# Optimization experiments

Hardware: AMD Instinct MI355X
Metric: run time of the kernel (lower is better)

Reference implementation:

```python
import jax, jax.numpy as jnp
import numpy as np
import math

B, N, D, H, T = 256, 512, 512, 8, 128
HD = D // H
CLIP = 10.0
CAP = 1.0
NEG = -1.0e9


def setup_inputs() -> dict:
    key = jax.random.key(0)
    ks = jax.random.split(key, 12)
    s = 1.0 / math.sqrt(D)
    return {
        "embeddings": jax.random.normal(ks[0], (B, N, D), jnp.float32),
        "mean_graph_emb": jax.random.normal(ks[1], (B, D), jnp.float32),
        "used_capacity": jax.random.uniform(ks[2], (T, B), jnp.float32),
        "Wk": jax.random.normal(ks[3], (D, D), jnp.float32) * s,
        "Wk_tanh": jax.random.normal(ks[4], (D, D), jnp.float32) * s,
        "Wv": jax.random.normal(ks[5], (D, D), jnp.float32) * s,
        "Wq_context": jax.random.normal(ks[6], (D, D), jnp.float32) * s,
        "Wq_step": jax.random.normal(ks[7], (D + 1, D), jnp.float32) * s,
        "Wout": jax.random.normal(ks[8], (D, D), jnp.float32) * s,
        "prev_a": jax.random.randint(ks[9], (T, B), 0, N, jnp.int32),
        "mask": jax.random.randint(ks[10], (T, B, N), 0, 2, jnp.int32),
    }


def reference(embeddings, mean_graph_emb, used_capacity, Wk, Wk_tanh, Wv,
              Wq_context, Wq_step, Wout, prev_a, mask):
    # Projections (done once per graph embedding, as in get_projections)
    K = (embeddings @ Wk).reshape(B, N, H, HD).transpose(0, 2, 1, 3)      # [B,H,N,hd]
    V = (embeddings @ Wv).reshape(B, N, H, HD).transpose(0, 2, 1, 3)      # [B,H,N,hd]
    K_tanh = embeddings @ Wk_tanh                                          # [B,N,D]
    Q_context = mean_graph_emb @ Wq_context                                # [B,D]

    inv_sqrt_hd = 1.0 / math.sqrt(HD)
    inv_sqrt_d = 1.0 / math.sqrt(D)

    def step(carry, xs):
        prev_t, cap_t, mask_t = xs  # [B], [B], [B,N]
        # get_step_context: gather prev node embedding + remaining capacity
        cur_emb = jnp.take_along_axis(embeddings, prev_t[:, None, None], axis=1)[:, 0]  # [B,D]
        step_ctx = jnp.concatenate([cur_emb, (CAP - cap_t)[:, None]], axis=-1)          # [B,D+1]
        q = Q_context + step_ctx @ Wq_step                                               # [B,D]
        qh = q.reshape(B, H, HD)                                                          # [B,H,hd]
        # decoder MHA, seq_len_q = 1
        logits = jnp.einsum("bhd,bhnd->bhn", qh, K) * inv_sqrt_hd                        # [B,H,N]
        logits = jnp.where(mask_t[:, None, :] == 1, NEG, logits)
        attn = jax.nn.softmax(logits, axis=-1)
        mha = jnp.einsum("bhn,bhnd->bhd", attn, V).reshape(B, D) @ Wout                  # [B,D]
        # single-head tanh-clipped pointer logits
        comp = jnp.einsum("bd,bnd->bn", mha, K_tanh) * inv_sqrt_d                        # [B,N]
        comp = jnp.tanh(comp) * CLIP
        comp = jnp.where(mask_t == 1, NEG, comp)
        p = jax.nn.softmax(comp, axis=-1)                                                # [B,N]
        return carry, p

    _, ps = jax.lax.scan(step, None, (prev_a, used_capacity, mask))  # [T,B,N]
    return ps.transpose(1, 0, 2)  # [B,T,N]
```

## Files before the change

### kernel.cpp

```cpp
#include <hip/hip_runtime.h>
#include <hip/hip_bf16.h>

constexpr int Bb = 256;
constexpr int Nn = 512;
constexpr int Dd = 512;
constexpr int Hh = 8;
constexpr int Tt = 128;
#define NEGF (-1.0e9f)

typedef __attribute__((ext_vector_type(4))) float f32x4;
typedef __attribute__((ext_vector_type(8))) short bf16x8;
typedef __attribute__((ext_vector_type(8))) unsigned short u16x8;

#define AS1 __attribute__((address_space(1)))
#define AS3 __attribute__((address_space(3)))

__device__ __forceinline__ unsigned short f2bf(float f) {
  union { float f; unsigned u; } v; v.f = f;
  unsigned r = v.u + 0x7fffu + ((v.u >> 16) & 1u);
  return (unsigned short)(r >> 16);
}

__device__ __forceinline__ unsigned cvtpk(float lo, float hi) {
  unsigned r;
  asm("v_cvt_pk_bf16_f32 %0, %1, %2" : "=v"(r) : "v"(lo), "v"(hi));
  return r;
}

__device__ __forceinline__ void cast8(const float* __restrict__ src,
                                      unsigned short* __restrict__ dst, int i) {
  const float4* s = (const float4*)src + (size_t)i * 2;
  float4 a = s[0], b = s[1];
  u16x8 o;
  o[0] = f2bf(a.x); o[1] = f2bf(a.y); o[2] = f2bf(a.z); o[3] = f2bf(a.w);
  o[4] = f2bf(b.x); o[5] = f2bf(b.y); o[6] = f2bf(b.z); o[7] = f2bf(b.w);
  ((u16x8*)dst)[i] = o;
}

__global__ void prep_k(const float* __restrict__ emb, const int* __restrict__ mask,
                       const float* __restrict__ Wkt, const float* __restrict__ Wout,
                       const float* __restrict__ mge,
                       const float* __restrict__ Wk, const float* __restrict__ Wv,
                       const float* __restrict__ Wqs, const float* __restrict__ Wqc,
                       unsigned short* __restrict__ embB, unsigned* __restrict__ bits,
                       unsigned short* __restrict__ WktB, unsigned short* __restrict__ WoutB,
                       unsigned short* __restrict__ mgeB,
                       unsigned short* __restrict__ WkT, unsigned short* __restrict__ WvT,
                       unsigned short* __restrict__ WqsT, unsigned short* __restrict__ WqcT) {
  __shared__ float t[32][33];
  int bid = blockIdx.x, tid = threadIdx.x;
  if (bid < 32768) {
    cast8(emb, embB, bid * 256 + tid);
  } else if (bid < 98304) {
    size_t gid = (size_t)(bid - 32768) * 256 + tid;
    int mv = mask[gid];
    unsigned long long bal = __ballot(mv == 1);
    if ((tid & 63) == 0) {
      unsigned tt = (unsigned)(gid >> 17);
      unsigned b = (unsigned)((gid >> 9) & 255);
      unsigned n = (unsigned)(gid & 511);
      unsigned* dst = bits + (((size_t)b * 128 + tt) * 16 + (n >> 5));
      dst[0] = (unsigned)bal;
      dst[1] = (unsigned)(bal >> 32);
    }
  } else if (bid < 98432) {
    cast8(Wkt, WktB, (bid - 98304) * 256 + tid);
  } else if (bid < 98560) {
    cast8(Wout, WoutB, (bid - 98432) * 256 + tid);
  } else if (bid < 98624) {
    cast8(mge, mgeB, (bid - 98560) * 256 + tid);
  } else {
    int vb = bid - 98624;
    int mid = vb >> 8;
    int tile = vb & 255;
    const float* S = (mid == 0) ? Wk : (mid == 1) ? Wv : (mid == 2) ? Wqs : Wqc;
    unsigned short* Dst = (mid == 0) ? WkT : (mid == 1) ? WvT : (mid == 2) ? WqsT : WqcT;
    int r0 = (tile >> 4) * 32, c0 = (tile & 15) * 32;
    int tx = tid & 31, ty = tid >> 5;
#pragma unroll
    for (int yy = 0; yy < 4; ++yy) {
      int r = ty + yy * 8;
      t[r][tx] = S[(size_t)(r0 + r) * 512 + c0 + tx];
    }
    __syncthreads();
#pragma unroll
    for (int yy = 0; yy < 4; ++yy) {
      int c = ty + yy * 8;
      Dst[(size_t)(c0 + c) * 512 + r0 + tx] = f2bf(t[tx][c]);
    }
  }
}

__device__ __forceinline__ void stage_tile(const unsigned short* __restrict__ G, int row0, int k0,
                                           unsigned short* lds_base, int wave, int lane) {
#pragma unroll
  for (int c = 0; c < 4; ++c) {
    int chunk = wave * 4 + c;
    const unsigned short* g = G + (size_t)(row0 + chunk * 8 + (lane >> 3)) * 512 + k0 + (lane & 7) * 8;
    __builtin_amdgcn_global_load_lds((AS1 void*)g, (AS3 void*)(lds_base + chunk * 512), 16, 0, 0);
  }
}

__global__ __launch_bounds__(256, 2)
void wfqc_k(const unsigned short* __restrict__ A0, const unsigned short* __restrict__ BT0,
            unsigned short* __restrict__ C0,
            const unsigned short* __restrict__ A1, const unsigned short* __restrict__ BT1,
            float* __restrict__ C1) {
  __shared__ __align__(16) char lds[32768];
  unsigned short* ldsA = (unsigned short*)lds;
  unsigned short* ldsB = ldsA + 8192;
  int bid = blockIdx.x;
  bool qc = (bid >= 16);
  int lb = qc ? bid - 16 : bid;
  const unsigned short* A = qc ? A1 : A0;
  const unsigned short* BT = qc ? BT1 : BT0;
  int mt = lb >> 2, nt = lb & 3;
  int m0 = mt * 128, n0 = nt * 128;
  int tid = threadIdx.x, lane = tid & 63, w = tid >> 6;
  int wm = w >> 1, wn = w & 1;
  int l15 = lane & 15, l4 = lane >> 4;

  f32x4 acc[4][4] = {};
  for (int k0 = 0; k0 < 512; k0 += 64) {
    stage_tile(A, m0, k0, ldsA, w, lane);
    stage_tile(BT, n0, k0, ldsB, w, lane);
    __syncthreads();
#pragma unroll
    for (int ks = 0; ks < 2; ++ks) {
      bf16x8 fa[4], fb[4];
#pragma unroll
      for (int ii = 0; ii < 4; ++ii)
        fa[ii] = *(const bf16x8*)(ldsA + (wm * 64 + ii * 16 + l15) * 64 + ks * 32 + l4 * 8);
#pragma unroll
      for (int jj = 0; jj < 4; ++jj)
        fb[jj] = *(const bf16x8*)(ldsB + (wn * 64 + jj * 16 + l15) * 64 + ks * 32 + l4 * 8);
#pragma unroll
      for (int ii = 0; ii < 4; ++ii)
#pragma unroll
        for (int jj = 0; jj < 4; ++jj)
          acc[ii][jj] = __builtin_amdgcn_mfma_f32_16x16x32_bf16(fa[ii], fb[jj], acc[ii][jj], 0, 0, 0);
    }
    __syncthreads();
  }
#pragma unroll
  for (int ii = 0; ii < 4; ++ii)
#pragma unroll
    for (int jj = 0; jj < 4; ++jj)
#pragma unroll
      for (int r = 0; r < 4; ++r) {
        int row = m0 + wm * 64 + ii * 16 + l4 * 4 + r;
        int col = n0 + wn * 64 + jj * 16 + l15;
        if (qc) C1[(size_t)row * 512 + col] = acc[ii][jj][r];
        else C0[(size_t)row * 512 + col] = f2bf(acc[ii][jj][r]);
      }
}

#define LDA_Q(QM)                                                   \
  _Pragma("unroll")                                                 \
  for (int ii = 0; ii < 4; ++ii) {                                  \
    int rr_ = (QM) * 64 + ii * 16 + l15;                            \
    const char* ap_ = ldsAh + rr_ * 128;                            \
    int sw_ = (rr_ & 7) << 4;                                       \
    fa[ii][0] = *(const bf16x8*)(ap_ + ((l4 * 16) ^ sw_));          \
    fa[ii][1] = *(const bf16x8*)(ap_ + ((64 + l4 * 16) ^ sw_));     \
  }

#define LDB_Q(QN)                                                   \
  _Pragma("unroll")                                                 \
  for (int jj = 0; jj < 2; ++jj) {                                  \
    int rr_ = (wn & 1) * 64 + (QN) * 32 + jj * 16 + l15;            \
    const char* bp_ = ldsBh + rr_ * 128;                            \
    int sw_ = (rr_ & 7) << 4;                                       \
    fb[jj][0] = *(const bf16x8*)(bp_ + ((l4 * 16) ^ sw_));          \
    fb[jj][1] = *(const bf16x8*)(bp_ + ((64 + l4 * 16) ^ sw_));     \
  }

#define MM16(QM, QN)                                                              \
  do {                                                                            \
    __builtin_amdgcn_s_setprio(1);                                                \
    _Pragma("unroll")                                                             \
    for (int ii = 0; ii < 4; ++ii)                                                \
      _Pragma("unroll")                                                           \
      for (int jj = 0; jj < 2; ++jj) {                                            \
        acc[(QM) * 4 + ii][(QN) * 2 + jj] = __builtin_amdgcn_mfma_f32_16x16x32_bf16( \
            fa[ii][0], fb[jj][0], acc[(QM) * 4 + ii][(QN) * 2 + jj], 0, 0, 0);    \
        acc[(QM) * 4 + ii][(QN) * 2 + jj] = __builtin_amdgcn_mfma_f32_16x16x32_bf16( \
            fa[ii][1], fb[jj][1], acc[(QM) * 4 + ii][(QN) * 2 + jj], 0, 0, 0);    \
      }                                                                           \
    __builtin_amdgcn_s_setprio(0);                                                \
  } while (0)

#define STAGE10A(SLOT, H, ROWB, KT)                                               \
  do {                                                                             \
    int rb_ = (ROWB) + (H) * 128;                                                  \
    char* Lb_ = lds + (SLOT) * 32768 + (H) * 16384;                                \
    _Pragma("unroll")                                                              \
    for (int sh_ = 0; sh_ < 2; ++sh_) {                                            \
      int off_ = sh_ * 8192 + tid * 16;                                            \
      int r_ = off_ >> 7;                                                          \
      int c_ = (off_ & 127) ^ ((r_ & 7) << 4);                                     \
      const char* g_ = (const char*)(A + (size_t)(rb_ + r_) * 512 + (KT) * 64) + c_; \
      __builtin_amdgcn_global_load_lds((AS1 void*)g_, (AS3 void*)(Lb_ + off_), 16, 0, 0); \
    }                                                                              \
  } while (0)

#define STAGE10B(SLOT, H, KT)                                                      \
  do {                                                                             \
    int rb_ = n0 + (H) * 128;                                                      \
    char* Lb_ = lds + 98304 + (SLOT) * 32768 + (H) * 16384;                        \
    _Pragma("unroll")                                                              \
    for (int sh_ = 0; sh_ < 2; ++sh_) {                                            \
      int off_ = sh_ * 8192 + tid * 16;                                            \
      int r_ = off_ >> 7;                                                          \
      int c_ = (off_ & 127) ^ ((r_ & 7) << 4);                                     \
      const char* g_ = (const char*)(BT + (size_t)(rb_ + r_) * 512 + (KT) * 64) + c_; \
      __builtin_amdgcn_global_load_lds((AS1 void*)g_, (AS3 void*)(Lb_ + off_), 16, 0, 0); \
    }                                                                              \
  } while (0)

#define STAGE11A(SLOT, H, KT)                                                      \
  do {                                                                             \
    char* Lb_ = lds + (SLOT) * 65536 + (H) * 16384;                                \
    __builtin_amdgcn_global_load_lds((AS1 void*)(abase[(H) * 2 + 0] + (KT) * 128), \
        (AS3 void*)(Lb_ + tid * 16), 16, 0, 0);                                    \
    __builtin_amdgcn_global_load_lds((AS1 void*)(abase[(H) * 2 + 1] + (KT) * 128), \
        (AS3 void*)(Lb_ + 8192 + tid * 16), 16, 0, 0);                             \
  } while (0)

#define STAGE11B(SLOT, H, KT)                                                      \
  do {                                                                             \
    int rb_ = n0 + (H) * 128;                                                      \
    char* Lb_ = lds + (SLOT) * 65536 + 32768 + (H) * 16384;                        \
    _Pragma("unroll")                                                              \
    for (int sh_ = 0; sh_ < 2; ++sh_) {                                            \
      int off_ = sh_ * 8192 + tid * 16;                                            \
      int r_ = off_ >> 7;                                                          \
      int c_ = (off_ & 127) ^ ((r_ & 7) << 4);                                     \
      const char* g_ = (const char*)(BT + (size_t)(rb_ + r_) * 512 + (KT) * 64) + c_; \
      __builtin_amdgcn_global_load_lds((AS1 void*)g_, (AS3 void*)(Lb_ + off_), 16, 0, 0); \
    }                                                                              \
  } while (0)

__global__ __launch_bounds__(512, 1)
void gemmq_k(const unsigned short* __restrict__ embB,
             const unsigned short* __restrict__ WqsT,
             unsigned short* __restrict__ Qb,
             const float* __restrict__ Qc, const float* __restrict__ WqsL,
             const float* __restrict__ capp, const int* __restrict__ prev,
             const unsigned short* __restrict__ B0, const unsigned short* __restrict__ B1,
             unsigned short* __restrict__ C0, unsigned short* __restrict__ C2) {
  __shared__ __align__(16) char lds[163840];
  int tid = threadIdx.x, lane = tid & 63, w = tid >> 6;
  int l15 = lane & 15, l4 = lane >> 4;

  if (blockIdx.x < 256) {
    const unsigned short* A = embB;
    const unsigned short* BT = WqsT;
    int xcd = blockIdx.x & 7, loc = blockIdx.x >> 3;
    int mt = xcd * 16 + (loc >> 1), nh = loc & 1;
    int m0 = mt * 256, n0 = nh * 256;
    int wm = w >> 2, wn = w & 3;

    const char* abase[4];
#pragma unroll
    for (int hs = 0; hs < 4; ++hs) {
      int H = hs >> 1, sh = hs & 1;
      int off = sh * 8192 + tid * 16;
      int r = off >> 7;
      int c = (off & 127) ^ ((r & 7) << 4);
      int row = m0 + H * 128 + r;
      int t = row >> 8, bb = row & 255;
      int pa = prev[t * Bb + bb];
      abase[hs] = (const char*)(A + (size_t)(bb * 512 + pa) * 512) + c;
    }

    f32x4 acc[8][4] = {};
    bf16x8 fa[4][2], fb[2][2];

    STAGE11A(0, 0, 0); STAGE11A(0, 1, 0);
    STAGE11B(0, 0, 0); STAGE11B(0, 1, 0);

    for (int kt = 0; kt < 8; ++kt) {
      int s = kt & 1, sn = s ^ 1;
      char* ldsAh = lds + s * 65536 + wm * 16384;
      char* ldsBh = lds + s * 65536 + 32768 + (wn >> 1) * 16384;
      if (kt < 7) {
        STAGE11A(sn, 0, kt + 1);
        asm volatile("s_waitcnt vmcnt(2)" ::: "memory");
      } else {
        asm volatile("s_waitcnt vmcnt(0)" ::: "memory");
      }
      __builtin_amdgcn_s_barrier();
      LDA_Q(0); LDB_Q(0);
      MM16(0, 0);
      __builtin_amdgcn_s_barrier();
      LDB_Q(1);
      if (kt < 7) STAGE11A(sn, 1, kt + 1);
      __builtin_amdgcn_s_barrier();
      MM16(0, 1);
      __builtin_amdgcn_s_barrier();
      LDA_Q(1);
      if (kt < 7) STAGE11B(sn, 0, kt + 1);
      __builtin_amdgcn_s_barrier();
      MM16(1, 1);
      __builtin_amdgcn_s_barrier();
      LDB_Q(0);
      if (kt < 7) STAGE11B(sn, 1, kt + 1);
      __builtin_amdgcn_s_barrier();
      MM16(1, 0);
      __builtin_amdgcn_s_barrier();
    }

#pragma unroll
    for (int mi = 0; mi < 8; ++mi)
#pragma unroll
      for (int nj = 0; nj < 4; ++nj)
#pragma unroll
        for (int r = 0; r < 4; ++r) {
          int row = m0 + wm * 128 + mi * 16 + l4 * 4 + r;
          int col = n0 + wn * 64 + nj * 16 + l15;
          int t = row >> 8, bbx = row & 255;
          float val = acc[mi][nj][r] + Qc[(size_t)bbx * 512 + col] + (1.0f - capp[row]) * WqsL[col];
          Qb[(size_t)(bbx * 128 + t) * 512 + col] = f2bf(val * 0.125f);
        }
  } else {
    const unsigned short* A = embB;
    int bid = blockIdx.x - 256;
    int xcd = bid & 7, loc = bid >> 3;
    int ml4 = loc >> 2, cmb = loc & 3;
    int grp = cmb >> 1, nh = cmb & 1;
    const unsigned short* BT = grp ? B1 : B0;
    int mtb = xcd * 64 + ml4 * 4;
    int n0 = nh * 256;
    int wm = w >> 2, wn = w & 3;

    f32x4 acc[8][4] = {};
    bf16x8 fa[4][2], fb[2][2];

    {
      int m00 = mtb * 256;
      STAGE10A(0, 0, m00, 0); STAGE10A(0, 1, m00, 0);
      STAGE10A(1, 0, m00, 1); STAGE10A(1, 1, m00, 1);
      STAGE10B(0, 0, 0);      STAGE10B(0, 1, 0);
    }

    for (int g = 0; g < 32; ++g) {
      int As = g % 3, Astg = (g + 2) % 3;
      int Bs = g & 1, Bstg = Bs ^ 1;
      char* ldsAh = lds + As * 32768 + wm * 16384;
      char* ldsBh = lds + 98304 + Bs * 32768 + (wn >> 1) * 16384;
      int g2 = g + 2;
      int m0A = (mtb + (g2 >> 3)) * 256, ktA = g2 & 7;
      int ktB = (g + 1) & 7;
      if (g < 30) {
        STAGE10A(Astg, 0, m0A, ktA);
        asm volatile("s_waitcnt vmcnt(2)" ::: "memory");
      } else {
        asm volatile("s_waitcnt vmcnt(0)" ::: "memory");
      }
      __builtin_amdgcn_s_barrier();
      LDA_Q(0); LDB_Q(0);
      MM16(0, 0);
      __builtin_amdgcn_s_barrier();
      LDB_Q(1);
      if (g < 30) STAGE10A(Astg, 1, m0A, ktA);
      __builtin_amdgcn_s_barrier();
      MM16(0, 1);
      __builtin_amdgcn_s_barrier();
      LDA_Q(1);
      if (g < 31) STAGE10B(Bstg, 0, ktB);
      __builtin_amdgcn_s_barrier();
      MM16(1, 1);
      __builtin_amdgcn_s_barrier();
      LDB_Q(0);
      if (g < 31) STAGE10B(Bstg, 1, ktB);
      __builtin_amdgcn_s_barrier();
      MM16(1, 0);
      __builtin_amdgcn_s_barrier();

      if ((g & 7) == 7) {
        int m0cur = (mtb + (g >> 3)) * 256;
        if (grp == 0) {
#pragma unroll
          for (int mi = 0; mi < 8; ++mi)
#pragma unroll
            for (int nj = 0; nj < 4; ++nj)
#pragma unroll
              for (int r = 0; r < 4; ++r) {
                int row = m0cur + wm * 128 + mi * 16 + l4 * 4 + r;
                int col = n0 + wn * 64 + nj * 16 + l15;
                C0[(size_t)row * 512 + col] = f2bf(acc[mi][nj][r]);
              }
        } else {
          int bb = m0cur >> 9, nn0 = m0cur & 511;
          char* wb = lds + As * 32768 + w * 4096;
          int rdrow = lane >> 3, nseg = lane & 7;
#pragma unroll
          for (int p = 0; p < 8; ++p) {
            int nj = p >> 1;
            if ((l15 >> 3) == (p & 1)) {
              int rowL = l15 & 7;
#pragma unroll
              for (int mi = 0; mi < 8; ++mi) {
                ushort4 w4;
                w4.x = f2bf(acc[mi][nj][0]);
                w4.y = f2bf(acc[mi][nj][1]);
                w4.z = f2bf(acc[mi][nj][2]);
                w4.w = f2bf(acc[mi][nj][3]);
                *(ushort4*)(wb + rowL * 272 + (mi * 16 + l4 * 4) * 2) = w4;
              }
            }
            asm volatile("s_waitcnt lgkmcnt(0)" ::: "memory");
            u16x8 v0 = *(const u16x8*)(wb + rdrow * 272 + nseg * 16);
            u16x8 v1 = *(const u16x8*)(wb + rdrow * 272 + 128 + nseg * 16);
            int dglob = n0 + wn * 64 + p * 8 + rdrow;
            unsigned short* dp = C2 + (size_t)(bb * 512 + dglob) * 512 + nn0 + wm * 128;
            *(u16x8*)(dp + nseg * 8) = v0;
            *(u16x8*)(dp + 64 + nseg * 8) = v1;
            asm volatile("s_waitcnt lgkmcnt(0)" ::: "memory");
          }
        }
#pragma unroll
        for (int mi = 0; mi < 8; ++mi)
#pragma unroll
          for (int nj = 0; nj < 4; ++nj)
            acc[mi][nj] = (f32x4){0.f, 0.f, 0.f, 0.f};
        __syncthreads();
      }
    }
  }
}

__global__ __launch_bounds__(512, 1)
void gemm11_k(const unsigned short* __restrict__ A, const unsigned short* __restrict__ BT,
              unsigned short* __restrict__ C) {
  __shared__ __align__(16) char lds[131072];
  int xcd = blockIdx.x & 7, loc = blockIdx.x >> 3;
  int mt = xcd * 16 + (loc >> 1), nh = loc & 1;
  int m0 = mt * 256, n0 = nh * 256;
  int tid = threadIdx.x, lane = tid & 63, w = tid >> 6;
  int wm = w >> 2, wn = w & 3;
  int l15 = lane & 15, l4 = lane >> 4;

  const char* abase[4];
#pragma unroll
  for (int hs = 0; hs < 4; ++hs) {
    int H = hs >> 1, sh = hs & 1;
    int off = sh * 8192 + tid * 16;
    int r = off >> 7;
    int c = (off & 127) ^ ((r & 7) << 4);
    int row = m0 + H * 128 + r;
    abase[hs] = (const char*)(A + (size_t)row * 512) + c;
  }

  f32x4 acc[8][4] = {};
  bf16x8 fa[4][2], fb[2][2];

  STAGE11A(0, 0, 0); STAGE11A(0, 1, 0);
  STAGE11B(0, 0, 0); STAGE11B(0, 1, 0);

  for (int kt = 0; kt < 8; ++kt) {
    int s = kt & 1, sn = s ^ 1;
    char* ldsAh = lds + s * 65536 + wm * 16384;
    char* ldsBh = lds + s * 65536 + 32768 + (wn >> 1) * 16384;
    if (kt < 7) {
      STAGE11A(sn, 0, kt + 1);
      asm volatile("s_waitcnt vmcnt(2)" ::: "memory");
    } else {
      asm volatile("s_waitcnt vmcnt(0)" ::: "memory");
    }
    __builtin_amdgcn_s_barrier();
    LDA_Q(0); LDB_Q(0);
    MM16(0, 0);
    __builtin_amdgcn_s_barrier();
    LDB_Q(1);
    if (kt < 7) STAGE11A(sn, 1, kt + 1);
    __builtin_amdgcn_s_barrier();
    MM16(0, 1);
    __builtin_amdgcn_s_barrier();
    LDA_Q(1);
    if (kt < 7) STAGE11B(sn, 0, kt + 1);
    __builtin_amdgcn_s_barrier();
    MM16(1, 1);
    __builtin_amdgcn_s_barrier();
    LDB_Q(0);
    if (kt < 7) STAGE11B(sn, 1, kt + 1);
    __builtin_amdgcn_s_barrier();
    MM16(1, 0);
    __builtin_amdgcn_s_barrier();
  }

#pragma unroll
  for (int mi = 0; mi < 8; ++mi)
#pragma unroll
    for (int nj = 0; nj < 4; ++nj)
#pragma unroll
      for (int r = 0; r < 4; ++r) {
        int row = m0 + wm * 128 + mi * 16 + l4 * 4 + r;
        int col = n0 + wn * 64 + nj * 16 + l15;
        C[(size_t)row * 512 + col] = f2bf(acc[mi][nj][r]);
      }
}

#define STAGEK5(CH, SLOT)                                                          \
  do {                                                                             \
    _Pragma("unroll")                                                              \
    for (int sh_ = 0; sh_ < 2; ++sh_) {                                            \
      int off_ = sh_ * 8192 + tid * 16;                                            \
      int r_ = off_ >> 7;                                                          \
      int c_ = (off_ & 127) ^ ((r_ & 7) << 4);                                     \
      const char* g_ = (const char*)(Kb + (size_t)(b * 512 + (CH) * 128 + r_) * 512 + h * 64) + c_; \
      __builtin_amdgcn_global_load_lds((AS1 void*)g_, (AS3 void*)(lds + (SLOT) * 16384 + off_), 16, 0, 0); \
    }                                                                              \
  } while (0)

#define STAGEV5(CH, SLOT)                                                          \
  do {                                                                             \
    _Pragma("unroll")                                                              \
    for (int sh_ = 0; sh_ < 2; ++sh_) {                                            \
      int off_ = sh_ * 8192 + tid * 16;                                            \
      int r_ = off_ >> 8;                                                          \
      int c_ = (off_ & 255) ^ ((r_ & 7) << 4);                                     \
      const char* g_ = (const char*)(Vt + (size_t)(b * 512 + h * 64 + r_) * 512 + (CH) * 128) + c_; \
      __builtin_amdgcn_global_load_lds((AS1 void*)g_, (AS3 void*)(lds + 32768 + (SLOT) * 16384 + off_), 16, 0, 0); \
    }                                                                              \
  } while (0)

#define CHUNK5(CH)                                                                 \
  do {                                                                             \
    const char* Ks_ = lds + ((CH) & 1) * 16384;                                    \
    const char* Vs_ = lds + 32768 + ((CH) & 1) * 16384;                            \
    f32x4 sck[8];                                                                  \
    _Pragma("unroll")                                                              \
    for (int jj = 0; jj < 8; ++jj) sck[jj] = (f32x4){0.f, 0.f, 0.f, 0.f};          \
    _Pragma("unroll")                                                              \
    for (int jj = 0; jj < 8; ++jj) {                                               \
      int rr_ = jj * 16 + l15;                                                     \
      int sw_ = (rr_ & 7) << 4;                                                    \
      bf16x8 k0_ = *(const bf16x8*)(Ks_ + rr_ * 128 + ((l4 * 16) ^ sw_));          \
      bf16x8 k1_ = *(const bf16x8*)(Ks_ + rr_ * 128 + ((64 + l4 * 16) ^ sw_));     \
      sck[jj] = __builtin_amdgcn_mfma_f32_16x16x32_bf16(k0_, fq[0], sck[jj], 0, 0, 0); \
      sck[jj] = __builtin_amdgcn_mfma_f32_16x16x32_bf16(k1_, fq[1], sck[jj], 0, 0, 0); \
    }                                                                              \
    unsigned mwarr_[4] = {mqs[CH].x, mqs[CH].y, mqs[CH].z, mqs[CH].w};             \
    float cmx_ = -3.0e38f;                                                         \
    _Pragma("unroll")                                                              \
    for (int jj = 0; jj < 8; ++jj) {                                               \
      unsigned nib_ = mwarr_[jj >> 1] >> (((jj & 1) << 4) + (l4 << 2));            \
      _Pragma("unroll")                                                            \
      for (int r = 0; r < 4; ++r)                                                  \
        sck[jj][r] = ((nib_ >> r) & 1) ? NEGF : sck[jj][r];                        \
      float m01_ = fmaxf(sck[jj][0], sck[jj][1]);                                  \
      float m23_ = fmaxf(sck[jj][2], sck[jj][3]);                                  \
      cmx_ = fmaxf(cmx_, fmaxf(m01_, m23_));                                       \
    }                                                                              \
    cmx_ = fmaxf(cmx_, __shfl_xor(cmx_, 16));                                      \
    cmx_ = fmaxf(cmx_, __shfl_xor(cmx_, 32));                                      \
    float mn_ = fmaxf(mx, cmx_);                                                   \
    float al_ = __expf(mx - mn_);                                                  \
    sum *= al_;                                                                    \
    _Pragma("unroll")                                                              \
    for (int dj = 0; dj < 4; ++dj)                                                 \
      _Pragma("unroll")                                                            \
      for (int r = 0; r < 4; ++r) o[dj][r] *= al_;                                 \
    mx = mn_;                                                                      \
    _Pragma("unroll")                                                              \
    for (int jj = 0; jj < 8; ++jj) {                                               \
      _Pragma("unroll")                                                            \
      for (int r = 0; r < 4; ++r) sck[jj][r] = __expf(sck[jj][r] - mx);            \
      sum += (sck[jj][0] + sck[jj][1]) + (sck[jj][2] + sck[jj][3]);                \
    }                                                                              \
    _Pragma("unroll")                                                              \
    for (int g = 0; g < 4; ++g) {                                                  \
      unsigned a0_ = cvtpk(sck[2 * g][0], sck[2 * g][1]);                          \
      unsigned a1_ = cvtpk(sck[2 * g][2], sck[2 * g][3]);                          \
      unsigned b0_ = cvtpk(sck[2 * g + 1][0], sck[2 * g + 1][1]);                  \
      unsigned b1_ = cvtpk(sck[2 * g + 1][2], sck[2 * g + 1][3]);                  \
      unsigned wA0_ = __shfl(a0_, src0, 64), wB0_ = __shfl(b0_, src0, 64);         \
      unsigned wA1_ = __shfl(a1_, src0, 64), wB1_ = __shfl(b1_, src0, 64);         \
      unsigned wA2_ = __shfl(a0_, src2, 64), wB2_ = __shfl(b0_, src2, 64);         \
      unsigned wA3_ = __shfl(a1_, src2, 64), wB3_ = __shfl(b1_, src2, 64);         \
      union { unsigned u[4]; bf16x8 v; } pu_;                                      \
      pu_.u[0] = loh ? wA0_ : wB0_;                                                \
      pu_.u[1] = loh ? wA1_ : wB1_;                                                \
      pu_.u[2] = loh ? wA2_ : wB2_;                                                \
      pu_.u[3] = loh ? wA3_ : wB3_;                                                \
      _Pragma("unroll")                                                            \
      for (int dj = 0; dj < 4; ++dj) {                                             \
        int rr_ = dj * 16 + l15;                                                   \
        int sw_ = (rr_ & 7) << 4;                                                  \
        bf16x8 fv_ = *(const bf16x8*)(Vs_ + rr_ * 256 + ((g * 64 + l4 * 16) ^ sw_)); \
        o[dj] = __builtin_amdgcn_mfma_f32_16x16x32_bf16(fv_, pu_.v, o[dj], 0, 0, 0); \
      }                                                                            \
    }                                                                              \
  } while (0)

__global__ __launch_bounds__(512, 4)
void attn5_k(const unsigned short* __restrict__ Qb, const unsigned short* __restrict__ Kb,
             const unsigned short* __restrict__ Vt, const unsigned* __restrict__ mbits,
             unsigned short* __restrict__ mhaB) {
  __shared__ __align__(16) char lds[65536];
  int bid = blockIdx.x;
  int h = bid & 7, b = bid >> 3;
  int tid = threadIdx.x, lane = tid & 63, w = tid >> 6;
  int l15 = lane & 15, l4 = lane >> 4;
  int t = w * 16 + l15;

  bf16x8 fq[2];
#pragma unroll
  for (int ks = 0; ks < 2; ++ks)
    fq[ks] = *(const bf16x8*)(Qb + (size_t)(b * 128 + t) * 512 + h * 64 + ks * 32 + l4 * 8);
  uint4 mqs[4];
  {
    const uint4* mp = (const uint4*)(mbits + (((size_t)b * 128 + t) << 4));
    mqs[0] = mp[0]; mqs[1] = mp[1]; mqs[2] = mp[2]; mqs[3] = mp[3];
  }

  float mx = -3.0e38f, sum = 0.f;
  f32x4 o[4] = {};
  int src0 = l15 + ((l4 & 1) ? 32 : 0);
  int src2 = l15 + ((l4 & 1) ? 48 : 16);
  bool loh = (l4 < 2);

  STAGEK5(0, 0); STAGEV5(0, 0);
  STAGEK5(1, 1); STAGEV5(1, 1);
  asm volatile("s_waitcnt vmcnt(4)" ::: "memory");
  __builtin_amdgcn_s_barrier();
  CHUNK5(0);
  __builtin_amdgcn_s_barrier();
  STAGEK5(2, 0); STAGEV5(2, 0);
  asm volatile("s_waitcnt vmcnt(4)" ::: "memory");
  __builtin_amdgcn_s_barrier();
  CHUNK5(1);
  __builtin_amdgcn_s_barrier();
  STAGEK5(3, 1); STAGEV5(3, 1);
  asm volatile("s_waitcnt vmcnt(4)" ::: "memory");
  __builtin_amdgcn_s_barrier();
  CHUNK5(2);
  __builtin_amdgcn_s_barrier();
  asm volatile("s_waitcnt vmcnt(0)" ::: "memory");
  __builtin_amdgcn_s_barrier();
  CHUNK5(3);

  sum += __shfl_xor(sum, 16);
  sum += __shfl_xor(sum, 32);
  float inv = 1.0f / sum;
#pragma unroll
  for (int dj = 0; dj < 4; ++dj) {
    ushort4 w4;
    w4.x = f2bf(o[dj][0] * inv);
    w4.y = f2bf(o[dj][1] * inv);
    w4.z = f2bf(o[dj][2] * inv);
    w4.w = f2bf(o[dj][3] * inv);
    *(ushort4*)(mhaB + (size_t)(b * 128 + t) * 512 + h * 64 + dj * 16 + l4 * 4) = w4;
  }
}

#define STAGEC5(CH, SLOT)                                                          \
  do {                                                                             \
    _Pragma("unroll")                                                              \
    for (int ps_ = 0; ps_ < 4; ++ps_) {                                            \
      int off_ = ps_ * 8192 + tid * 16;                                            \
      int r_ = off_ >> 10;                                                         \
      int c_ = (off_ & 1023) ^ ((r_ & 7) << 4);                                    \
      const char* g_ = (const char*)(embB + (size_t)(b * 512 + nh * 256 + (CH) * 32 + r_) * 512) + c_; \
      __builtin_amdgcn_global_load_lds((AS1 void*)g_, (AS3 void*)(lds + (SLOT) * 32768 + off_), 16, 0, 0); \
    }                                                                              \
  } while (0)

#define CCHUNK5(CH)                                                                \
  do {                                                                             \
    const char* Es_ = lds + ((CH) & 1) * 32768;                                    \
    _Pragma("unroll")                                                              \
    for (int jjl_ = 0; jjl_ < 2; ++jjl_) {                                         \
      f32x4 sck = (f32x4){0.f, 0.f, 0.f, 0.f};                                     \
      int rr_ = jjl_ * 16 + l15;                                                   \
      const char* ep_ = Es_ + rr_ * 1024;                                          \
      int sw_ = (rr_ & 7) << 4;                                                    \
      _Pragma("unroll")                                                            \
      for (int ks_ = 0; ks_ < 16; ++ks_) {                                         \
        bf16x8 fa_ = *(const bf16x8*)(ep_ + ((ks_ * 64 + l4 * 16) ^ sw_));         \
        sck = __builtin_amdgcn_mfma_f32_16x16x32_bf16(fa_, fb[ks_], sck, 0, 0, 0); \
      }                                                                            \
      unsigned nib_ = mwh[CH] >> ((jjl_ << 4) + (l4 << 2));                        \
      float4 o4_;                                                                  \
      float* po_ = (float*)&o4_;                                                   \
      _Pragma("unroll")                                                            \
      for (int r = 0; r < 4; ++r) {                                                \
        float y_ = sck[r] * 0.044194173824159216f;                                 \
        y_ = fminf(fmaxf(y_, -15.f), 15.f);                                        \
        float e2_ = __expf(2.f * y_);                                              \
        float th_ = (e2_ - 1.f) / (e2_ + 1.f);                                     \
        float p_ = __expf(th_ * 10.f - 10.f);                                      \
        p_ = ((nib_ >> r) & 1) ? 0.f : p_;                                         \
        po_[r] = p_;                                                               \
        sum += p_;                                                                 \
      }                                                                            \
      *(float4*)(out + (size_t)(b * 128 + t) * 512 + nh * 256 + (CH) * 32 + jjl_ * 16 + l4 * 4) = o4_; \
    }                                                                              \
  } while (0)

__global__ __launch_bounds__(512, 2)
void comp5_k(const unsigned short* __restrict__ mh2, const unsigned short* __restrict__ embB,
             const unsigned* __restrict__ mbits, float* __restrict__ out,
             float* __restrict__ sums) {
  __shared__ __align__(16) char lds[65536];
  int b = blockIdx.x >> 1, nh = blockIdx.x & 1;
  int tid = threadIdx.x, lane = tid & 63, w = tid >> 6;
  int l15 = lane & 15, l4 = lane >> 4;
  int t = w * 16 + l15;

  bf16x8 fb[16];
#pragma unroll
  for (int ks = 0; ks < 16; ++ks)
    fb[ks] = *(const bf16x8*)(mh2 + (size_t)(b * 128 + t) * 512 + ks * 32 + l4 * 8);
  unsigned mwh[8];
  {
    const uint4* mp = (const uint4*)(mbits + (((size_t)b * 128 + t) << 4)) + nh * 2;
    uint4 a0 = mp[0], a1 = mp[1];
    mwh[0] = a0.x; mwh[1] = a0.y; mwh[2] = a0.z; mwh[3] = a0.w;
    mwh[4] = a1.x; mwh[5] = a1.y; mwh[6] = a1.z; mwh[7] = a1.w;
  }

  float sum = 0.f;
  STAGEC5(0, 0);
  STAGEC5(1, 1);
  asm volatile("s_waitcnt vmcnt(4)" ::: "memory");
  __builtin_amdgcn_s_barrier();
  CCHUNK5(0);
  __builtin_amdgcn_s_barrier();
  STAGEC5(2, 0);
  asm volatile("s_waitcnt vmcnt(4)" ::: "memory");
  __builtin_amdgcn_s_barrier();
  CCHUNK5(1);
  __builtin_amdgcn_s_barrier();
  STAGEC5(3, 1);
  asm volatile("s_waitcnt vmcnt(4)" ::: "memory");
  __builtin_amdgcn_s_barrier();
  CCHUNK5(2);
  __builtin_amdgcn_s_barrier();
  STAGEC5(4, 0);
  asm volatile("s_waitcnt vmcnt(4)" ::: "memory");
  __builtin_amdgcn_s_barrier();
  CCHUNK5(3);
  __builtin_amdgcn_s_barrier();
  STAGEC5(5, 1);
  asm volatile("s_waitcnt vmcnt(4)" ::: "memory");
  __builtin_amdgcn_s_barrier();
  CCHUNK5(4);
  __builtin_amdgcn_s_barrier();
  STAGEC5(6, 0);
  asm volatile("s_waitcnt vmcnt(4)" ::: "memory");
  __builtin_amdgcn_s_barrier();
  CCHUNK5(5);
  __builtin_amdgcn_s_barrier();
  STAGEC5(7, 1);
  asm volatile("s_waitcnt vmcnt(4)" ::: "memory");
  __builtin_amdgcn_s_barrier();
  CCHUNK5(6);
  __builtin_amdgcn_s_barrier();
  asm volatile("s_waitcnt vmcnt(0)" ::: "memory");
  __builtin_amdgcn_s_barrier();
  CCHUNK5(7);

  sum += __shfl_xor(sum, 16);
  sum += __shfl_xor(sum, 32);
  if (l4 == 0) sums[nh * 32768 + b * 128 + t] = sum;
}

__global__ void norm_k(float* __restrict__ out, const float* __restrict__ sums) {
  int row = blockIdx.x * 4 + (threadIdx.x >> 6);
  int lane = threadIdx.x & 63;
  float inv = 1.0f / (sums[row] + sums[32768 + row]);
  float4* p = (float4*)(out + (size_t)row * 512) + lane;
  float4 a = p[0], b = p[64];
  a.x *= inv; a.y *= inv; a.z *= inv; a.w *= inv;
  b.x *= inv; b.y *= inv; b.z *= inv; b.w *= inv;
  p[0] = a; p[64] = b;
}

extern "C" void kernel_launch(void* const* d_in, const int* in_sizes, int n_in,
                              void* d_out, int out_size, void* d_ws, size_t ws_size,
                              hipStream_t stream) {
  (void)in_sizes; (void)n_in; (void)out_size; (void)ws_size;
  const float* emb  = (const float*)d_in[0];
  const float* mge  = (const float*)d_in[1];
  const float* cap  = (const float*)d_in[2];
  const float* Wk   = (const float*)d_in[3];
  const float* Wkt  = (const float*)d_in[4];
  const float* Wv   = (const float*)d_in[5];
  const float* Wqc  = (const float*)d_in[6];
  const float* Wqs  = (const float*)d_in[7];
  const float* Wout = (const float*)d_in[8];
  const int* prev   = (const int*)d_in[9];
  const int* mask   = (const int*)d_in[10];
  float* out = (float*)d_out;

  char* p = (char*)d_ws;
  auto take = [&](size_t n) { char* q = p; p += (n + 255) & ~(size_t)255; return q; };
  unsigned short* embB = (unsigned short*)take((size_t)131072 * 512 * 2);
  unsigned short* Kb   = (unsigned short*)take((size_t)131072 * 512 * 2);
  unsigned short* Vt   = (unsigned short*)take((size_t)131072 * 512 * 2);
  unsigned short* Qb   = (unsigned short*)take((size_t)32768 * 512 * 2);
  unsigned short* mhaB = (unsigned short*)take((size_t)32768 * 512 * 2);
  unsigned short* mh2  = (unsigned short*)take((size_t)32768 * 512 * 2);
  float*          Qc   = (float*)take((size_t)256 * 512 * 4);
  unsigned*       mbit = (unsigned*)take((size_t)256 * 128 * 16 * 4);
  float*          sums = (float*)take((size_t)2 * 32768 * 4);
  unsigned short* WkT  = (unsigned short*)take(524288);
  unsigned short* WvT  = (unsigned short*)take(524288);
  unsigned short* WqsT = (unsigned short*)take(524288);
  unsigned short* WqcT = (unsigned short*)take(524288);
  unsigned short* WktB = (unsigned short*)take(524288);
  unsigned short* WoutB= (unsigned short*)take(524288);
  unsigned short* WFT  = (unsigned short*)take(524288);
  unsigned short* mgeB = (unsigned short*)take((size_t)256 * 512 * 2);

  prep_k<<<99648, 256, 0, stream>>>(emb, mask, Wkt, Wout, mge, Wk, Wv, Wqs, Wqc,
                                    embB, mbit, WktB, WoutB, mgeB, WkT, WvT, WqsT, WqcT);
  wfqc_k<<<24, 256, 0, stream>>>(WktB, WoutB, WFT, mgeB, WqcT, Qc);
  gemmq_k<<<768, 512, 0, stream>>>(embB, WqsT, Qb, Qc, Wqs + 512 * 512, cap, prev,
                                   WkT, WvT, Kb, Vt);
  attn5_k<<<2048, 512, 0, stream>>>(Qb, Kb, Vt, mbit, mhaB);
  gemm11_k<<<256, 512, 0, stream>>>(mhaB, WFT, mh2);
  comp5_k<<<512, 512, 0, stream>>>(mh2, embB, mbit, out, sums);
  norm_k<<<8192, 256, 0, stream>>>(out, sums);
}
```

Measured before the change: 487.1 us.

## Fuse softmax normalization into pointer-logit kernel by splitting blocks over time

The pointer-logit kernel now splits work across blocks by time-step halves instead of node halves, so each thread sees the full row of N logits. It can then compute the complete softmax sum itself and rescale its own output row in place, which removes the separate norm kernel and the sums buffer. The cost is that each block now streams all 512 embedding rows per batch through a 32-chunk rolled loop with smaller LDS tiles. The rescale pass re-reads and re-writes the output row from global memory within the same kernel.

```diff
diff --git a/kernel.cpp b/kernel.cpp
--- a/kernel.cpp
+++ b/kernel.cpp
@@ -656,127 +656,101 @@
   }
 }
 
-#define STAGEC5(CH, SLOT)                                                          \
+#define STAGEC6(CH, SLOT)                                                          \
   do {                                                                             \
     _Pragma("unroll")                                                              \
     for (int ps_ = 0; ps_ < 4; ++ps_) {                                            \
-      int off_ = ps_ * 8192 + tid * 16;                                            \
+      int off_ = ps_ * 4096 + tid * 16;                                            \
       int r_ = off_ >> 10;                                                         \
       int c_ = (off_ & 1023) ^ ((r_ & 7) << 4);                                    \
-      const char* g_ = (const char*)(embB + (size_t)(b * 512 + nh * 256 + (CH) * 32 + r_) * 512) + c_; \
-      __builtin_amdgcn_global_load_lds((AS1 void*)g_, (AS3 void*)(lds + (SLOT) * 32768 + off_), 16, 0, 0); \
-    }                                                                              \
-  } while (0)
-
-#define CCHUNK5(CH)                                                                \
+      const char* g_ = (const char*)(embB + (size_t)(b * 512 + (CH) * 16 + r_) * 512) + c_; \
+      __builtin_amdgcn_global_load_lds((AS1 void*)g_, (AS3 void*)(lds + (SLOT) * 16384 + off_), 16, 0, 0); \
+    }                                                                              \
+  } while (0)
+
+#define CCHUNK6(CH)                                                               \
   do {                                                                             \
-    const char* Es_ = lds + ((CH) & 1) * 32768;                                    \
-    _Pragma("unroll")                                                              \
-    for (int jjl_ = 0; jjl_ < 2; ++jjl_) {                                         \
-      f32x4 sck = (f32x4){0.f, 0.f, 0.f, 0.f};                                     \
-      int rr_ = jjl_ * 16 + l15;                                                   \
-      const char* ep_ = Es_ + rr_ * 1024;                                          \
-      int sw_ = (rr_ & 7) << 4;                                                    \
-      _Pragma("unroll")                                                            \
-      for (int ks_ = 0; ks_ < 16; ++ks_) {                                         \
-        bf16x8 fa_ = *(const bf16x8*)(ep_ + ((ks_ * 64 + l4 * 16) ^ sw_));         \
-        sck = __builtin_amdgcn_mfma_f32_16x16x32_bf16(fa_, fb[ks_], sck, 0, 0, 0); \
-      }                                                                            \
-      unsigned nib_ = mwh[CH] >> ((jjl_ << 4) + (l4 << 2));                        \
-      float4 o4_;                                                                  \
-      float* po_ = (float*)&o4_;                                                   \
-      _Pragma("unroll")                                                            \
-      for (int r = 0; r < 4; ++r) {                                                \
-        float y_ = sck[r] * 0.044194173824159216f;                                 \
-        y_ = fminf(fmaxf(y_, -15.f), 15.f);                                        \
-        float e2_ = __expf(2.f * y_);                                              \
-        float th_ = (e2_ - 1.f) / (e2_ + 1.f);                                     \
-        float p_ = __expf(th_ * 10.f - 10.f);                                      \
-        p_ = ((nib_ >> r) & 1) ? 0.f : p_;                                         \
-        po_[r] = p_;                                                               \
-        sum += p_;                                                                 \
-      }                                                                            \
-      *(float4*)(out + (size_t)(b * 128 + t) * 512 + nh * 256 + (CH) * 32 + jjl_ * 16 + l4 * 4) = o4_; \
-    }                                                                              \
-  } while (0)
-
-__global__ __launch_bounds__(512, 2)
-void comp5_k(const unsigned short* __restrict__ mh2, const unsigned short* __restrict__ embB,
-             const unsigned* __restrict__ mbits, float* __restrict__ out,
-             float* __restrict__ sums) {
-  __shared__ __align__(16) char lds[65536];
-  int b = blockIdx.x >> 1, nh = blockIdx.x & 1;
+    const char* Es_ = lds + ((CH) & 1) * 16384;                                    \
+    f32x4 sck = (f32x4){0.f, 0.f, 0.f, 0.f};                                       \
+    int rr_ = l15;                                                                 \
+    const char* ep_ = Es_ + rr_ * 1024;                                            \
+    int sw_ = (rr_ & 7) << 4;                                                      \
+    _Pragma("unroll")                                                              \
+    for (int ks_ = 0; ks_ < 16; ++ks_) {                                           \
+      bf16x8 fa_ = *(const bf16x8*)(ep_ + ((ks_ * 64 + l4 * 16) ^ sw_));           \
+      sck = __builtin_amdgcn_mfma_f32_16x16x32_bf16(fa_, fb[ks_], sck, 0, 0, 0);   \
+    }                                                                              \
+    unsigned nib_ = mw[(CH) >> 1] >> ((((CH) & 1) << 4) + (l4 << 2));              \
+    float4 o4_;                                                                    \
+    float* po_ = (float*)&o4_;                                                     \
+    _Pragma("unroll")                                                              \
+    for (int r = 0; r < 4; ++r) {                                                  \
+      float y_ = sck[r] * 0.044194173824159216f;                                   \
+      y_ = fminf(fmaxf(y_, -15.f), 15.f);                                          \
+      float e2_ = __expf(2.f * y_);                                                \
+      float th_ = (e2_ - 1.f) / (e2_ + 1.f);                                       \
+      float p_ = __expf(th_ * 10.f - 10.f);                                        \
+      p_ = ((nib_ >> r) & 1) ? 0.f : p_;                                           \
+      po_[r] = p_;                                                                 \
+      sum += p_;                                                                   \
+    }                                                                              \
+    *(float4*)(out + (size_t)(b * 128 + t) * 512 + (CH) * 16 + l4 * 4) = o4_;      \
+  } while (0)
+
+__global__ __launch_bounds__(256, 4)
+void comp6_k(const unsigned short* __restrict__ mh2, const unsigned short* __restrict__ embB,
+             const unsigned* __restrict__ mbits, float* __restrict__ out) {
+  __shared__ __align__(16) char lds[32768];
+  int b = blockIdx.x & 255, th = blockIdx.x >> 8;
   int tid = threadIdx.x, lane = tid & 63, w = tid >> 6;
   int l15 = lane & 15, l4 = lane >> 4;
-  int t = w * 16 + l15;
+  int t = th * 64 + w * 16 + l15;
 
   bf16x8 fb[16];
 #pragma unroll
   for (int ks = 0; ks < 16; ++ks)
     fb[ks] = *(const bf16x8*)(mh2 + (size_t)(b * 128 + t) * 512 + ks * 32 + l4 * 8);
-  unsigned mwh[8];
+  unsigned mw[16];
   {
-    const uint4* mp = (const uint4*)(mbits + (((size_t)b * 128 + t) << 4)) + nh * 2;
-    uint4 a0 = mp[0], a1 = mp[1];
-    mwh[0] = a0.x; mwh[1] = a0.y; mwh[2] = a0.z; mwh[3] = a0.w;
-    mwh[4] = a1.x; mwh[5] = a1.y; mwh[6] = a1.z; mwh[7] = a1.w;
+    const uint4* mp = (const uint4*)(mbits + (((size_t)b * 128 + t) << 4));
+    uint4 a0 = mp[0], a1 = mp[1], a2 = mp[2], a3 = mp[3];
+    mw[0] = a0.x; mw[1] = a0.y; mw[2] = a0.z; mw[3] = a0.w;
+    mw[4] = a1.x; mw[5] = a1.y; mw[6] = a1.z; mw[7] = a1.w;
+    mw[8] = a2.x; mw[9] = a2.y; mw[10] = a2.z; mw[11] = a2.w;
+    mw[12] = a3.x; mw[13] = a3.y; mw[14] = a3.z; mw[15] = a3.w;
   }
 
   float sum = 0.f;
-  STAGEC5(0, 0);
-  STAGEC5(1, 1);
+  STAGEC6(0, 0);
+  STAGEC6(1, 1);
   asm volatile("s_waitcnt vmcnt(4)" ::: "memory");
   __builtin_amdgcn_s_barrier();
-  CCHUNK5(0);
+  CCHUNK6(0);
   __builtin_amdgcn_s_barrier();
-  STAGEC5(2, 0);
-  asm volatile("s_waitcnt vmcnt(4)" ::: "memory");
-  __builtin_amdgcn_s_barrier();
-  CCHUNK5(1);
-  __builtin_amdgcn_s_barrier();
-  STAGEC5(3, 1);
-  asm volatile("s_waitcnt vmcnt(4)" ::: "memory");
-  __builtin_amdgcn_s_barrier();
-  CCHUNK5(2);
-  __builtin_amdgcn_s_barrier();
-  STAGEC5(4, 0);
-  asm volatile("s_waitcnt vmcnt(4)" ::: "memory");
-  __builtin_amdgcn_s_barrier();
-  CCHUNK5(3);
-  __builtin_amdgcn_s_barrier();
-  STAGEC5(5, 1);
-  asm volatile("s_waitcnt vmcnt(4)" ::: "memory");
-  __builtin_amdgcn_s_barrier();
-  CCHUNK5(4);
-  __builtin_amdgcn_s_barrier();
-  STAGEC5(6, 0);
-  asm volatile("s_waitcnt vmcnt(4)" ::: "memory");
-  __builtin_amdgcn_s_barrier();
-  CCHUNK5(5);
-  __builtin_amdgcn_s_barrier();
-  STAGEC5(7, 1);
-  asm volatile("s_waitcnt vmcnt(4)" ::: "memory");
-  __builtin_amdgcn_s_barrier();
-  CCHUNK5(6);
-  __builtin_amdgcn_s_barrier();
-  asm volatile("s_waitcnt vmcnt(0)" ::: "memory");
-  __builtin_amdgcn_s_barrier();
-  CCHUNK5(7);
+  for (int ch = 1; ch < 32; ++ch) {
+    if (ch < 31) {
+      STAGEC6(ch + 1, (ch + 1) & 1);
+      asm volatile("s_waitcnt vmcnt(4)" ::: "memory");
+    } else {
+      asm volatile("s_waitcnt vmcnt(0)" ::: "memory");
+    }
+    __builtin_amdgcn_s_barrier();
+    CCHUNK6(ch);
+    __builtin_amdgcn_s_barrier();
+  }
 
   sum += __shfl_xor(sum, 16);
   sum += __shfl_xor(sum, 32);
-  if (l4 == 0) sums[nh * 32768 + b * 128 + t] = sum;
-}
-
-__global__ void norm_k(float* __restrict__ out, const float* __restrict__ sums) {
-  int row = blockIdx.x * 4 + (threadIdx.x >> 6);
-  int lane = threadIdx.x & 63;
-  float inv = 1.0f / (sums[row] + sums[32768 + row]);
-  float4* p = (float4*)(out + (size_t)row * 512) + lane;
-  float4 a = p[0], b = p[64];
-  a.x *= inv; a.y *= inv; a.z *= inv; a.w *= inv;
-  b.x *= inv; b.y *= inv; b.z *= inv; b.w *= inv;
-  p[0] = a; p[64] = b;
+  float inv = 1.0f / sum;
+
+  asm volatile("s_waitcnt vmcnt(0)" ::: "memory");
+  float4* rp = (float4*)(out + (size_t)(b * 128 + t) * 512 + l4 * 128);
+#pragma unroll
+  for (int i = 0; i < 32; ++i) {
+    float4 v = rp[i];
+    v.x *= inv; v.y *= inv; v.z *= inv; v.w *= inv;
+    rp[i] = v;
+  }
 }
 
 extern "C" void kernel_launch(void* const* d_in, const int* in_sizes, int n_in,
@@ -806,7 +780,6 @@
   unsigned short* mh2  = (unsigned short*)take((size_t)32768 * 512 * 2);
   float*          Qc   = (float*)take((size_t)256 * 512 * 4);
   unsigned*       mbit = (unsigned*)take((size_t)256 * 128 * 16 * 4);
-  float*          sums = (float*)take((size_t)2 * 32768 * 4);
   unsigned short* WkT  = (unsigned short*)take(524288);
   unsigned short* WvT  = (unsigned short*)take(524288);
   unsigned short* WqsT = (unsigned short*)take(524288);
@@ -823,6 +796,5 @@
                                    WkT, WvT, Kb, Vt);
   attn5_k<<<2048, 512, 0, stream>>>(Qb, Kb, Vt, mbit, mhaB);
   gemm11_k<<<256, 512, 0, stream>>>(mhaB, WFT, mh2);
-  comp5_k<<<512, 512, 0, stream>>>(mh2, embB, mbit, out, sums);
-  norm_k<<<8192, 256, 0, stream>>>(out, sums);
-}
+  comp6_k<<<512, 256, 0, stream>>>(mh2, embB, mbit, out);
+}
```

New measurement: 496.9 us. 1.02x slower.
